# Optimization experiments

Measured on AMD Instinct MI355X. Metric: run time of the kernel, lower is better.

Reference implementation:

```python
import jax, jax.numpy as jnp
import numpy as np

B, N, FIN, FOUT = 8, 2048, 128, 64
ALPHA = 0.2      # LeakyReLU negative slope
NEG_INF = -9e15  # matches torch constant -9000000000000000.0
LN_EPS = 1e-5


def setup_inputs() -> dict:
    key = jax.random.key(0)
    k1, k2, k3, k4 = jax.random.split(key, 4)
    x = jax.random.normal(k1, (B, N, FIN), dtype=jnp.float32)
    adj = jax.random.randint(k2, (B, N, N), 0, 2, dtype=jnp.int32)
    # params: W is nn.Linear(in,out,bias=False) -> stored here as [FIN,FOUT];
    # a is nn.Linear(2*out,1,bias=False) -> vector of length 2*FOUT.
    W = jax.random.normal(k3, (FIN, FOUT), dtype=jnp.float32) * (1.0 / np.sqrt(FIN))
    a = jax.random.normal(k4, (2 * FOUT,), dtype=jnp.float32) * (1.0 / np.sqrt(2 * FOUT))
    gamma = jnp.ones((FOUT,), dtype=jnp.float32)
    beta = jnp.zeros((FOUT,), dtype=jnp.float32)
    return {"x": x, "adj": adj, "W": W, "a": a, "gamma": gamma, "beta": beta}


def reference(x, adj, W, a, gamma, beta):
    h = jnp.einsum('bnf,fo->bno', x, W)                      # [B,N,FOUT]
    fout = h.shape[-1]
    a1, a2 = a[:fout], a[fout:]
    # a·cat(h_i,h_j) == h_i·a1 + h_j·a2 -> avoid O(N^2*2F) concat tensor
    s1 = h @ a1                                              # [B,N]
    s2 = h @ a2                                              # [B,N]
    e = jax.nn.leaky_relu(s1[:, :, None] + s2[:, None, :], ALPHA)  # [B,N,N]
    att = jnp.where(adj > 0, e, NEG_INF)
    att = jax.nn.softmax(att, axis=2)
    h_prime = jnp.einsum('bij,bjf->bif', att, h)             # [B,N,FOUT]
    # LayerNorm over last dim
    mu = jnp.mean(h_prime, axis=-1, keepdims=True)
    var = jnp.mean((h_prime - mu) ** 2, axis=-1, keepdims=True)
    y = (h_prime - mu) * jax.lax.rsqrt(var + LN_EPS) * gamma + beta
    return jax.nn.elu(y)
```

## Files before the change

### kernel.cpp

```cpp
#include <hip/hip_runtime.h>
#include <hip/hip_bf16.h>

#define B_    8
#define N_    2048
#define FIN_  128
#define FOUT_ 64
#define ALPHA_ 0.2f
#define LN_EPS_ 1e-5f

typedef __attribute__((ext_vector_type(8))) short short8;
typedef __attribute__((ext_vector_type(4))) float f32x4;

__device__ __forceinline__ short f2bf(float f) {
    __hip_bfloat16 h = __float2bfloat16(f);
    return *reinterpret_cast<short*>(&h);
}
__device__ __forceinline__ float bf2f(short s) {
    return __uint_as_float(((unsigned)(unsigned short)s) << 16);
}

__global__ __launch_bounds__(256) void k_proj(
    const float* __restrict__ x,
    const float* __restrict__ W,
    const float* __restrict__ a,
    unsigned short* __restrict__ hT,
    float* __restrict__ s1, float* __restrict__ s2)
{
    __shared__ short Wb[16 * 64 * 8];
    __shared__ float Wa1l[FIN_], Wa2l[FIN_];
    const int t = threadIdx.x;
    const int row0 = blockIdx.x * 32;
    const int b   = row0 >> 11;
    const int ib0 = row0 & (N_ - 1);

    #pragma unroll
    for (int c = 0; c < 4; ++c) {
        int g = t + 256 * c;
        int u = g >> 6, ln = g & 63;
        int ks = u >> 2, nt = u & 3;
        int n  = nt * 16 + (ln & 15);
        int k0 = ks * 32 + (ln >> 4) * 8;
        short8 v;
        #pragma unroll
        for (int jj = 0; jj < 8; ++jj) v[jj] = f2bf(W[(k0 + jj) * FOUT_ + n]);
        *(short8*)&Wb[g * 8] = v;
    }
    if (t < FIN_) {
        float a1 = 0.f, a2 = 0.f;
        #pragma unroll
        for (int n = 0; n < FOUT_; n += 4) {
            float4 wv  = *(const float4*)&W[t * FOUT_ + n];
            float4 av1 = *(const float4*)&a[n];
            float4 av2 = *(const float4*)&a[FOUT_ + n];
            a1 += wv.x * av1.x + wv.y * av1.y + wv.z * av1.z + wv.w * av1.w;
            a2 += wv.x * av2.x + wv.y * av2.y + wv.z * av2.z + wv.w * av2.w;
        }
        Wa1l[t] = a1; Wa2l[t] = a2;
    }
    __syncthreads();

    const int wave = t >> 6, lane = t & 63;
    const int m = lane & 15, quad = lane >> 4;
    const int mt = wave & 1, nt0 = (wave >> 1) * 2;
    const int row = row0 + mt * 16 + m;

    short8 fa[4];
    float s1p = 0.f, s2p = 0.f;
    #pragma unroll
    for (int ks = 0; ks < 4; ++ks) {
        int k0 = ks * 32 + quad * 8;
        float4 x0 = *(const float4*)&x[(size_t)row * FIN_ + k0];
        float4 x1 = *(const float4*)&x[(size_t)row * FIN_ + k0 + 4];
        float xs[8] = {x0.x, x0.y, x0.z, x0.w, x1.x, x1.y, x1.z, x1.w};
        short8 v;
        #pragma unroll
        for (int jj = 0; jj < 8; ++jj) {
            v[jj] = f2bf(xs[jj]);
            s1p += xs[jj] * Wa1l[k0 + jj];
            s2p += xs[jj] * Wa2l[k0 + jj];
        }
        fa[ks] = v;
    }
    s1p += __shfl_xor(s1p, 16); s1p += __shfl_xor(s1p, 32);
    s2p += __shfl_xor(s2p, 16); s2p += __shfl_xor(s2p, 32);
    if (wave < 2 && lane < 16) {
        s1[row0 + wave * 16 + lane] = s1p;
        s2[row0 + wave * 16 + lane] = s2p;
    }

    f32x4 acc[2];
    acc[0] = (f32x4){0.f, 0.f, 0.f, 0.f};
    acc[1] = (f32x4){0.f, 0.f, 0.f, 0.f};
    #pragma unroll
    for (int ks = 0; ks < 4; ++ks) {
        #pragma unroll
        for (int q = 0; q < 2; ++q) {
            short8 fb = *(short8*)&Wb[((ks * 4 + nt0 + q) * 64 + lane) * 8];
            acc[q] = __builtin_amdgcn_mfma_f32_16x16x32_bf16(fa[ks], fb, acc[q], 0, 0, 0);
        }
    }
    #pragma unroll
    for (int q = 0; q < 2; ++q) {
        int o  = (nt0 + q) * 16 + m;
        int ib = ib0 + mt * 16 + quad * 4;
        ushort4 hv;
        hv.x = (unsigned short)f2bf(acc[q][0]);
        hv.y = (unsigned short)f2bf(acc[q][1]);
        hv.z = (unsigned short)f2bf(acc[q][2]);
        hv.w = (unsigned short)f2bf(acc[q][3]);
        *(ushort4*)&hT[(size_t)(b * 64 + o) * N_ + ib] = hv;
    }
}

__global__ __launch_bounds__(256) void k_attn(
    const int* __restrict__ adj,
    const unsigned short* __restrict__ hT,
    const float* __restrict__ s1g, const float* __restrict__ s2g,
    const float* __restrict__ gamma, const float* __restrict__ beta,
    float* __restrict__ out)
{
    __shared__ float s2l[N_];
    __shared__ float accL[4][16][64];
    __shared__ float lpw[4][16];
    __shared__ float red[4];

    const int t = threadIdx.x;
    const int wave = t >> 6, lane = t & 63;
    const int i_ = lane & 15, quad = lane >> 4;
    const int b  = blockIdx.x >> 7;
    const int i0 = (blockIdx.x & 127) * 16;
    const size_t sbase = (size_t)b * N_;
    const size_t hTb   = (size_t)b * 64 * N_;

    float4 v0 = *(const float4*)&s2g[sbase + 4 * t];
    float4 v1 = *(const float4*)&s2g[sbase + 4 * (t + 256)];
    *(float4*)&s2l[4 * t] = v0;
    *(float4*)&s2l[4 * (t + 256)] = v1;
    float mx = fmaxf(fmaxf(fmaxf(v0.x, v0.y), fmaxf(v0.z, v0.w)),
                     fmaxf(fmaxf(v1.x, v1.y), fmaxf(v1.z, v1.w)));
    #pragma unroll
    for (int d = 32; d; d >>= 1) mx = fmaxf(mx, __shfl_xor(mx, d));
    if (lane == 0) red[wave] = mx;
    __syncthreads();
    const float smax = fmaxf(fmaxf(red[0], red[1]), fmaxf(red[2], red[3]));
    const float s1v  = s1g[sbase + i0 + i_];
    const float mv   = fmaxf(s1v + smax, ALPHA_ * (s1v + smax));

    const int jr = wave * 32 + quad * 8;
    const int* adjrow = &adj[(sbase + i0 + i_) * N_ + jr];

    int4 pa0 = *(const int4*)&adjrow[0];
    int4 pa1 = *(const int4*)&adjrow[4];

    f32x4 acc[4];
    #pragma unroll
    for (int nt = 0; nt < 4; ++nt) acc[nt] = (f32x4){0.f, 0.f, 0.f, 0.f};
    float lpart = 0.f;

    for (int tile = 0; tile < 16; ++tile) {
        const int j0 = tile * 128;
        int am[8] = {pa0.x, pa0.y, pa0.z, pa0.w, pa1.x, pa1.y, pa1.z, pa1.w};

        {
            int jn = ((tile + 1) & 15) * 128;
            pa0 = *(const int4*)&adjrow[jn];
            pa1 = *(const int4*)&adjrow[jn + 4];
        }
        short8 hv[4];
        #pragma unroll
        for (int nt = 0; nt < 4; ++nt)
            hv[nt] = *(const short8*)&hT[hTb + (size_t)(nt * 16 + i_) * N_ + j0 + jr];

        short8 wv;
        {
            float sum = 0.f;
            #pragma unroll
            for (int jj = 0; jj < 8; ++jj) {
                float ev = s1v + s2l[j0 + jr + jj];
                ev = fmaxf(ev, ALPHA_ * ev);
                float w = (am[jj] > 0) ? __expf(ev - mv) : 0.f;
                short ws = f2bf(w);
                wv[jj] = ws;
                sum += bf2f(ws);
            }
            lpart += sum;
        }

        #pragma unroll
        for (int nt = 0; nt < 4; ++nt)
            acc[nt] = __builtin_amdgcn_mfma_f32_16x16x32_bf16(wv, hv[nt], acc[nt], 0, 0, 0);
    }

    lpart += __shfl_xor(lpart, 16);
    lpart += __shfl_xor(lpart, 32);
    if (lane < 16) lpw[wave][lane] = lpart;

    #pragma unroll
    for (int nt = 0; nt < 4; ++nt)
        #pragma unroll
        for (int reg = 0; reg < 4; ++reg)
            accL[wave][nt * 4 + reg][lane] = acc[nt][reg];
    __syncthreads();

    {
        const int o = lane, ntc = o >> 4, oc = o & 15;
        const float g  = gamma[o];
        const float be = beta[o];
        #pragma unroll
        for (int rr = 0; rr < 4; ++rr) {
            int i = wave * 4 + rr;
            int s = ntc * 4 + (i & 3), lp = (i >> 2) * 16 + oc;
            float c = accL[0][s][lp] + accL[1][s][lp] + accL[2][s][lp] + accL[3][s][lp];
            float l = lpw[0][i] + lpw[1][i] + lpw[2][i] + lpw[3][i];
            float v = c / l;
            float mu = v;
            #pragma unroll
            for (int d = 32; d; d >>= 1) mu += __shfl_xor(mu, d);
            mu *= (1.f / 64.f);
            float dv = v - mu;
            float var = dv * dv;
            #pragma unroll
            for (int d = 32; d; d >>= 1) var += __shfl_xor(var, d);
            var *= (1.f / 64.f);
            float y = dv * rsqrtf(var + LN_EPS_) * g + be;
            out[(sbase + i0 + i) * FOUT_ + o] = y > 0.f ? y : __expf(y) - 1.f;
        }
    }
}

extern "C" void kernel_launch(void* const* d_in, const int* in_sizes, int n_in,
                              void* d_out, int out_size, void* d_ws, size_t ws_size,
                              hipStream_t stream) {
    const float* x     = (const float*)d_in[0];
    const int*   adj   = (const int*)d_in[1];
    const float* W     = (const float*)d_in[2];
    const float* a     = (const float*)d_in[3];
    const float* gamma = (const float*)d_in[4];
    const float* beta  = (const float*)d_in[5];
    float* out = (float*)d_out;

    char* ws = (char*)d_ws;
    unsigned short* hT = (unsigned short*)ws;
    float* s1 = (float*)(ws + (size_t)B_ * 64 * N_ * 2);
    float* s2 = s1 + (size_t)B_ * N_;

    k_proj<<<512, 256, 0, stream>>>(x, W, a, hT, s1, s2);
    k_attn<<<B_ * (N_ / 16), 256, 0, stream>>>(adj, hT, s1, s2, gamma, beta, out);
}
```

Baseline: 226.3 us.

## Double-buffer attention tiles, use exp2 with prescaled scores, packed bf16 converts

Processes two 128-column tiles per iteration of the attention loop. Adjacency prefetch doubles and the h loads of the second tile are issued before the first tile's MFMAs, so load latency overlaps the exp math. The attention-score projections are prescaled by log2(e) so the kernel can call exp2f directly, and s2 is read from shared memory as float4. Float-to-bf16 conversions now use packed two-wide intrinsics. The softmax denominator is now summed from the unrounded fp32 weights instead of the bf16-rounded values, which slightly changes numerics and adds register pressure.

```diff
diff --git a/kernel.cpp b/kernel.cpp
--- a/kernel.cpp
+++ b/kernel.cpp
@@ -7,16 +7,14 @@
 #define FOUT_ 64
 #define ALPHA_ 0.2f
 #define LN_EPS_ 1e-5f
+#define LOG2E_ 1.4426950408889634f
 
 typedef __attribute__((ext_vector_type(8))) short short8;
 typedef __attribute__((ext_vector_type(4))) float f32x4;
 
-__device__ __forceinline__ short f2bf(float f) {
-    __hip_bfloat16 h = __float2bfloat16(f);
-    return *reinterpret_cast<short*>(&h);
-}
-__device__ __forceinline__ float bf2f(short s) {
-    return __uint_as_float(((unsigned)(unsigned short)s) << 16);
+__device__ __forceinline__ short2 pk_bf(float a, float b) {
+    __hip_bfloat162 h = __float22bfloat162_rn(float2{a, b});
+    return *reinterpret_cast<short2*>(&h);
 }
 
 __global__ __launch_bounds__(256) void k_proj(
@@ -42,7 +40,10 @@
         int k0 = ks * 32 + (ln >> 4) * 8;
         short8 v;
         #pragma unroll
-        for (int jj = 0; jj < 8; ++jj) v[jj] = f2bf(W[(k0 + jj) * FOUT_ + n]);
+        for (int jj = 0; jj < 8; jj += 2) {
+            short2 p = pk_bf(W[(k0 + jj) * FOUT_ + n], W[(k0 + jj + 1) * FOUT_ + n]);
+            v[jj] = p.x; v[jj + 1] = p.y;
+        }
         *(short8*)&Wb[g * 8] = v;
     }
     if (t < FIN_) {
@@ -55,7 +56,7 @@
             a1 += wv.x * av1.x + wv.y * av1.y + wv.z * av1.z + wv.w * av1.w;
             a2 += wv.x * av2.x + wv.y * av2.y + wv.z * av2.z + wv.w * av2.w;
         }
-        Wa1l[t] = a1; Wa2l[t] = a2;
+        Wa1l[t] = a1 * LOG2E_; Wa2l[t] = a2 * LOG2E_;
     }
     __syncthreads();
 
@@ -74,8 +75,12 @@
         float xs[8] = {x0.x, x0.y, x0.z, x0.w, x1.x, x1.y, x1.z, x1.w};
         short8 v;
         #pragma unroll
+        for (int jj = 0; jj < 8; jj += 2) {
+            short2 p = pk_bf(xs[jj], xs[jj + 1]);
+            v[jj] = p.x; v[jj + 1] = p.y;
+        }
+        #pragma unroll
         for (int jj = 0; jj < 8; ++jj) {
-            v[jj] = f2bf(xs[jj]);
             s1p += xs[jj] * Wa1l[k0 + jj];
             s2p += xs[jj] * Wa2l[k0 + jj];
         }
@@ -103,11 +108,11 @@
     for (int q = 0; q < 2; ++q) {
         int o  = (nt0 + q) * 16 + m;
         int ib = ib0 + mt * 16 + quad * 4;
+        short2 p0 = pk_bf(acc[q][0], acc[q][1]);
+        short2 p1 = pk_bf(acc[q][2], acc[q][3]);
         ushort4 hv;
-        hv.x = (unsigned short)f2bf(acc[q][0]);
-        hv.y = (unsigned short)f2bf(acc[q][1]);
-        hv.z = (unsigned short)f2bf(acc[q][2]);
-        hv.w = (unsigned short)f2bf(acc[q][3]);
+        hv.x = (unsigned short)p0.x; hv.y = (unsigned short)p0.y;
+        hv.z = (unsigned short)p1.x; hv.w = (unsigned short)p1.y;
         *(ushort4*)&hT[(size_t)(b * 64 + o) * N_ + ib] = hv;
     }
 }
@@ -151,44 +156,84 @@
 
     int4 pa0 = *(const int4*)&adjrow[0];
     int4 pa1 = *(const int4*)&adjrow[4];
+    int4 pb0 = *(const int4*)&adjrow[128];
+    int4 pb1 = *(const int4*)&adjrow[132];
 
     f32x4 acc[4];
     #pragma unroll
     for (int nt = 0; nt < 4; ++nt) acc[nt] = (f32x4){0.f, 0.f, 0.f, 0.f};
     float lpart = 0.f;
 
-    for (int tile = 0; tile < 16; ++tile) {
-        const int j0 = tile * 128;
-        int am[8] = {pa0.x, pa0.y, pa0.z, pa0.w, pa1.x, pa1.y, pa1.z, pa1.w};
-
+    #pragma unroll 2
+    for (int it = 0; it < 8; ++it) {
+        const int j0 = it * 256;
+        int am0[8] = {pa0.x, pa0.y, pa0.z, pa0.w, pa1.x, pa1.y, pa1.z, pa1.w};
+        int am1[8] = {pb0.x, pb0.y, pb0.z, pb0.w, pb1.x, pb1.y, pb1.z, pb1.w};
         {
-            int jn = ((tile + 1) & 15) * 128;
+            int jn = ((it + 1) & 7) * 256;
             pa0 = *(const int4*)&adjrow[jn];
             pa1 = *(const int4*)&adjrow[jn + 4];
-        }
-        short8 hv[4];
-        #pragma unroll
-        for (int nt = 0; nt < 4; ++nt)
-            hv[nt] = *(const short8*)&hT[hTb + (size_t)(nt * 16 + i_) * N_ + j0 + jr];
-
-        short8 wv;
+            pb0 = *(const int4*)&adjrow[jn + 128];
+            pb1 = *(const int4*)&adjrow[jn + 132];
+        }
+
+        short8 hv0[4];
+        #pragma unroll
+        for (int nt = 0; nt < 4; ++nt)
+            hv0[nt] = *(const short8*)&hT[hTb + (size_t)(nt * 16 + i_) * N_ + j0 + jr];
+        short8 wv0;
         {
-            float sum = 0.f;
+            float4 sa = *(const float4*)&s2l[j0 + jr];
+            float4 sb = *(const float4*)&s2l[j0 + jr + 4];
+            float sv[8] = {sa.x, sa.y, sa.z, sa.w, sb.x, sb.y, sb.z, sb.w};
+            float w[8];
             #pragma unroll
             for (int jj = 0; jj < 8; ++jj) {
-                float ev = s1v + s2l[j0 + jr + jj];
+                float ev = s1v + sv[jj];
                 ev = fmaxf(ev, ALPHA_ * ev);
-                float w = (am[jj] > 0) ? __expf(ev - mv) : 0.f;
-                short ws = f2bf(w);
-                wv[jj] = ws;
-                sum += bf2f(ws);
-            }
-            lpart += sum;
-        }
-
-        #pragma unroll
-        for (int nt = 0; nt < 4; ++nt)
-            acc[nt] = __builtin_amdgcn_mfma_f32_16x16x32_bf16(wv, hv[nt], acc[nt], 0, 0, 0);
+                float e = exp2f(ev - mv);
+                w[jj] = (am0[jj] > 0) ? e : 0.f;
+                lpart += w[jj];
+            }
+            #pragma unroll
+            for (int jj = 0; jj < 8; jj += 2) {
+                short2 p = pk_bf(w[jj], w[jj + 1]);
+                wv0[jj] = p.x; wv0[jj + 1] = p.y;
+            }
+        }
+
+        short8 hv1[4];
+        #pragma unroll
+        for (int nt = 0; nt < 4; ++nt)
+            hv1[nt] = *(const short8*)&hT[hTb + (size_t)(nt * 16 + i_) * N_ + j0 + 128 + jr];
+
+        #pragma unroll
+        for (int nt = 0; nt < 4; ++nt)
+            acc[nt] = __builtin_amdgcn_mfma_f32_16x16x32_bf16(wv0, hv0[nt], acc[nt], 0, 0, 0);
+
+        short8 wv1;
+        {
+            float4 sa = *(const float4*)&s2l[j0 + 128 + jr];
+            float4 sb = *(const float4*)&s2l[j0 + 128 + jr + 4];
+            float sv[8] = {sa.x, sa.y, sa.z, sa.w, sb.x, sb.y, sb.z, sb.w};
+            float w[8];
+            #pragma unroll
+            for (int jj = 0; jj < 8; ++jj) {
+                float ev = s1v + sv[jj];
+                ev = fmaxf(ev, ALPHA_ * ev);
+                float e = exp2f(ev - mv);
+                w[jj] = (am1[jj] > 0) ? e : 0.f;
+                lpart += w[jj];
+            }
+            #pragma unroll
+            for (int jj = 0; jj < 8; jj += 2) {
+                short2 p = pk_bf(w[jj], w[jj + 1]);
+                wv1[jj] = p.x; wv1[jj + 1] = p.y;
+            }
+        }
+        #pragma unroll
+        for (int nt = 0; nt < 4; ++nt)
+            acc[nt] = __builtin_amdgcn_mfma_f32_16x16x32_bf16(wv1, hv1[nt], acc[nt], 0, 0, 0);
     }
 
     lpart += __shfl_xor(lpart, 16);
```

Measured after the change: 228.8 us. No clear change (+1.1%).
